# Kernel optimization log

Measured on AMD Instinct MI355X. Metric: run time of the kernel, lower is better.

Reference implementation:

```python
import jax, jax.numpy as jnp
import numpy as np

NUM_HEADS = 16
HEAD_DIM = 64  # hidden_size 1024 / 16 heads


def setup_inputs() -> dict:
    key = jax.random.key(0)
    ks = jax.random.split(key, 4)
    B, S, H = 2, 2048, 1024
    scale = 0.02
    return {
        "hidden_states": jax.random.normal(ks[0], (B, S, H), jnp.float32),
        "attention_mask": jnp.zeros((B, 1, 1, S), jnp.float32),  # additive mask
        "Wq": jax.random.normal(ks[1], (H, H), jnp.float32) * scale,
        "bq": jnp.zeros((H,), jnp.float32),
        "Wk": jax.random.normal(ks[2], (H, H), jnp.float32) * scale,
        "bk": jnp.zeros((H,), jnp.float32),
        "Wv": jax.random.normal(ks[3], (H, H), jnp.float32) * scale,
        "bv": jnp.zeros((H,), jnp.float32),
    }


def _split_heads(x):
    B, S, H = x.shape
    return x.reshape(B, S, NUM_HEADS, HEAD_DIM).transpose(0, 2, 1, 3)  # [B,h,S,dh]


def reference(hidden_states, attention_mask, Wq, bq, Wk, bk, Wv, bv):
    q = _split_heads(hidden_states @ Wq + bq)
    k = _split_heads(hidden_states @ Wk + bk)
    v = _split_heads(hidden_states @ Wv + bv)
    # scaled dot-product scores [B,h,S,S]
    scores = jnp.einsum("bhqd,bhkd->bhqk", q, k) / np.sqrt(HEAD_DIM).astype(np.float32)
    scores = scores + attention_mask  # additive mask, broadcast [B,1,1,S]
    probs = jax.nn.softmax(scores, axis=-1)  # dropout prob = 0.0
    ctx = jnp.einsum("bhqk,bhkd->bhqd", probs, v)
    B, h, S, dh = ctx.shape
    return ctx.transpose(0, 2, 1, 3).reshape(B, S, h * dh)  # [B,S,hidden]
```

## Files before the change

### kernel.cpp

```cpp
#include <hip/hip_runtime.h>
#include <hip/hip_bf16.h>


typedef __bf16 bf16x8 __attribute__((ext_vector_type(8)));
typedef __bf16 bf16x4 __attribute__((ext_vector_type(4)));
typedef float f32x4 __attribute__((ext_vector_type(4)));
typedef float f32x16 __attribute__((ext_vector_type(16)));
typedef int i32x4 __attribute__((ext_vector_type(4)));

static constexpr int H = 1024;
static constexpr int S = 2048;
static constexpr int NH = 16;
static constexpr int DH = 64;
static constexpr float L2E = 1.4426950408889634f;

#if __has_builtin(__builtin_amdgcn_exp2f)
#define EXP2F(x) __builtin_amdgcn_exp2f(x)
#else
#define EXP2F(x) __builtin_exp2f(x)
#endif

__device__ inline void gll16(const void* g, void* l) {
  __builtin_amdgcn_global_load_lds(
      (const __attribute__((address_space(1))) void*)g,
      (__attribute__((address_space(3))) void*)l, 16, 0, 0);
}

__device__ inline int pack2bf(float lo, float hi) {
  unsigned short a = __builtin_bit_cast(unsigned short, (__bf16)lo);
  unsigned short b = __builtin_bit_cast(unsigned short, (__bf16)hi);
  return (int)(((unsigned)b << 16) | (unsigned)a);
}

__device__ inline void plswap(int& a, int& b) {
  asm volatile("v_permlane32_swap_b32 %0, %1" : "+v"(a), "+v"(b));
}

__global__ __launch_bounds__(256) void convert_kernel(
    const float* __restrict__ X, const float* __restrict__ W0,
    const float* __restrict__ W1, const float* __restrict__ W2,
    __bf16* __restrict__ Xb, __bf16* __restrict__ Wt) {
  __shared__ float T[64][65];
  const int bid = blockIdx.x, tid = threadIdx.x;
  if (bid < 2048) {
    size_t i = ((size_t)bid * 256 + tid) * 8;
    float4 f0 = *(const float4*)(X + i);
    float4 f1 = *(const float4*)(X + i + 4);
    bf16x8 o;
    o[0] = (__bf16)f0.x; o[1] = (__bf16)f0.y; o[2] = (__bf16)f0.z; o[3] = (__bf16)f0.w;
    o[4] = (__bf16)f1.x; o[5] = (__bf16)f1.y; o[6] = (__bf16)f1.z; o[7] = (__bf16)f1.w;
    *(bf16x8*)(Xb + i) = o;
    return;
  }
  const int wid = bid - 2048;
  const int z = wid >> 8, t = wid & 255;
  const int k0 = (t >> 4) * 64, n0 = (t & 15) * 64;
  const float* W = z == 0 ? W0 : (z == 1 ? W1 : W2);
  __bf16* Wo = Wt + (size_t)z * H * H;
#pragma unroll
  for (int it = 0; it < 4; ++it) {
    int r = it * 16 + (tid >> 4), c = (tid & 15) * 4;
    *(float4*)&T[r][c] = *(const float4*)&W[(size_t)(k0 + r) * H + n0 + c];
  }
  __syncthreads();
#pragma unroll
  for (int it = 0; it < 4; ++it) {
    int n = it * 16 + (tid >> 4), c0 = (tid & 15) * 4;
    bf16x4 o;
#pragma unroll
    for (int j = 0; j < 4; ++j) o[j] = (__bf16)T[c0 + j][n];
    *(bf16x4*)&Wo[(size_t)(n0 + n) * H + k0 + c0] = o;
  }
}

__global__ __launch_bounds__(256, 3) void qkv_gemm_kernel(
    const __bf16* __restrict__ Xb, const __bf16* __restrict__ Wt,
    const float* __restrict__ bq, const float* __restrict__ bk,
    const float* __restrict__ bv,
    __bf16* __restrict__ Qt, __bf16* __restrict__ K, __bf16* __restrict__ Vt)
{
  __shared__ __bf16 As[128 * 64];
  __shared__ __bf16 Bs[128 * 64];

  const int tid = threadIdx.x, lane = tid & 63, w = tid >> 6;
  const int quad = lane >> 4, l16 = lane & 15;

  const int lin = blockIdx.x + 24 * blockIdx.y;
  const int swz = (lin & 7) * 96 + (lin >> 3);
  const int bx = swz >> 5;
  const int by = swz & 31;
  const int wsel = bx >> 3;
  const int n0 = (bx & 7) * 128;
  const int m0 = by * 128;
  const int wr = w & 1, wc = w >> 1;

  const __bf16* Wsel = Wt + (size_t)wsel * H * H;
  const float* bias = wsel == 0 ? bq : (wsel == 1 ? bk : bv);

  const __bf16* aptr[4];
  const __bf16* bptr[4];
#pragma unroll
  for (int i = 0; i < 4; ++i) {
    int s = w * 256 + i * 64 + lane;
    int row = s >> 3, col = s & 7, sc = col ^ (row & 7);
    aptr[i] = Xb + (size_t)(m0 + row) * H + sc * 8;
    bptr[i] = Wsel + (size_t)(n0 + row) * H + sc * 8;
  }

  f32x4 acc[4][4] = {};

  for (int k0 = 0; k0 < H; k0 += 64) {
    __syncthreads();
#pragma unroll
    for (int i = 0; i < 4; ++i) {
      gll16(aptr[i] + k0, &As[(w * 256 + i * 64) * 8]);
      gll16(bptr[i] + k0, &Bs[(w * 256 + i * 64) * 8]);
    }
    __syncthreads();
#pragma unroll
    for (int kc = 0; kc < 2; ++kc) {
      bf16x8 af[4], bfr[4];
#pragma unroll
      for (int t = 0; t < 4; ++t) {
        int ra = wr * 64 + t * 16 + l16;
        af[t] = *(const bf16x8*)&As[ra * 64 + (((kc * 4 + quad) ^ (ra & 7)) * 8)];
        int rb = wc * 64 + t * 16 + l16;
        bfr[t] = *(const bf16x8*)&Bs[rb * 64 + (((kc * 4 + quad) ^ (rb & 7)) * 8)];
      }
#pragma unroll
      for (int t = 0; t < 4; ++t)
#pragma unroll
        for (int u = 0; u < 4; ++u)
          acc[t][u] = __builtin_amdgcn_mfma_f32_16x16x32_bf16(af[t], bfr[u], acc[t][u], 0, 0, 0);
    }
  }

  const float qscale = 0.125f * L2E;
#pragma unroll
  for (int u = 0; u < 4; ++u) {
    int n = n0 + wc * 64 + u * 16 + l16;
    int head = n >> 6, d = n & 63;
    float bias_v = bias[n];
#pragma unroll
    for (int t = 0; t < 4; ++t) {
      int srow = m0 + wr * 64 + t * 16 + quad * 4;
      int b = srow >> 11, si = srow & (S - 1);
      int bh = b * NH + head;
      if (wsel == 1) {
        __bf16* dst = K + ((size_t)bh * S + si) * DH + d;
#pragma unroll
        for (int r = 0; r < 4; ++r)
          dst[(size_t)r * DH] = (__bf16)(acc[t][u][r] + bias_v);
      } else {
        float scl = wsel == 0 ? qscale : 1.0f;
        __bf16* outp = wsel == 0 ? Qt : Vt;
        bf16x4 o;
#pragma unroll
        for (int r = 0; r < 4; ++r) o[r] = (__bf16)((acc[t][u][r] + bias_v) * scl);
        *(bf16x4*)&outp[((size_t)bh * DH + d) * S + si] = o;
      }
    }
  }
}

__global__ __launch_bounds__(512, 4) void attn_kernel(
    const __bf16* __restrict__ Qt, const __bf16* __restrict__ K,
    const __bf16* __restrict__ Vt, const float* __restrict__ mask,
    float* __restrict__ out)
{
  __shared__ __bf16 SM[20480];
  __bf16* Ksb = SM;
  __bf16* Vsb = SM + 8192;
  float*  Ms  = (float*)(SM + 16384);

  const int tid = threadIdx.x, lane = tid & 63, w = tid >> 6;
  const int l31 = lane & 31, hi = lane >> 5;
  const int wl = w & 3, wh = w >> 2;

  const int lin = blockIdx.y * 16 + blockIdx.x;
  const int v = (lin & 7) * 64 + (lin >> 3);
  const int bh = v >> 4, b = bh >> 4, h = bh & 15;
  const int q0 = (v & 15) * 128;

  const __bf16* Qb = Qt + (size_t)bh * DH * S;
  const __bf16* Kb = K + (size_t)bh * S * DH;
  const __bf16* Vb = Vt + (size_t)bh * DH * S;
  const float* mb = mask + (size_t)b * S;

  {
    int idx = tid * 4;
    float4 mv = *(const float4*)&mb[idx];
    float4 sv = {mv.x * L2E, mv.y * L2E, mv.z * L2E, mv.w * L2E};
    *(float4*)&Ms[idx] = sv;
  }

  const int q = q0 + wl * 32 + l31;
  bf16x8 qf[4];
#pragma unroll
  for (int kc = 0; kc < 4; ++kc)
#pragma unroll
    for (int j = 0; j < 8; ++j)
      qf[kc][j] = Qb[(size_t)(kc * 16 + hi * 8 + j) * S + q];

  const int kvbase = wh * 1024;
  const __bf16* kptr[2];
  const __bf16* vptr[2];
#pragma unroll
  for (int i = 0; i < 2; ++i) {
    int s = wl * 128 + i * 64 + lane;
    int row = s >> 3, col = s & 7, sc = col ^ (row & 7);
    kptr[i] = Kb + (size_t)(kvbase + row) * DH + sc * 8;
    vptr[i] = Vb + (size_t)row * S + kvbase + sc * 8;
  }

  f32x16 o0 = {}, o1 = {};
  float dl = 0.0f;

  for (int st = 0; st < 16; ++st) {
    __syncthreads();
#pragma unroll
    for (int i = 0; i < 2; ++i) {
      gll16(kptr[i] + (size_t)st * 64 * DH,
            &Ksb[wh * 4096 + (wl * 128 + i * 64 + lane) * 8]);
      gll16(vptr[i] + st * 64,
            &Vsb[wh * 4096 + (wl * 128 + i * 64 + lane) * 8]);
    }
    __syncthreads();
    const __bf16* Kc = &Ksb[wh * 4096];
    const __bf16* Vc = &Vsb[wh * 4096];
    const int kvabs = kvbase + st * 64;

#pragma unroll
    for (int kvsub = 0; kvsub < 2; ++kvsub) {
      const int rk = kvsub * 32 + l31;
      f32x16 cc;
#pragma unroll
      for (int g = 0; g < 4; ++g) {
        float4 m4 = *(const float4*)&Ms[kvabs + kvsub * 32 + g * 8 + hi * 4];
        cc[4 * g + 0] = m4.x; cc[4 * g + 1] = m4.y;
        cc[4 * g + 2] = m4.z; cc[4 * g + 3] = m4.w;
      }
      __builtin_amdgcn_s_setprio(1);
#pragma unroll
      for (int kc = 0; kc < 4; ++kc) {
        bf16x8 af = *(const bf16x8*)&Kc[rk * 64 + (((kc * 2 + hi) ^ (l31 & 7)) * 8)];
        cc = __builtin_amdgcn_mfma_f32_32x32x16_bf16(af, qf[kc], cc, 0, 0, 0);
      }
      __builtin_amdgcn_s_setprio(0);

      float p[16];
#pragma unroll
      for (int r = 0; r < 16; ++r) { p[r] = EXP2F(cc[r]); dl += p[r]; }
      int a0 = pack2bf(p[0],  p[1]),  b0 = pack2bf(p[2],  p[3]);
      int a1 = pack2bf(p[4],  p[5]),  b1 = pack2bf(p[6],  p[7]);
      int a2 = pack2bf(p[8],  p[9]),  b2 = pack2bf(p[10], p[11]);
      int a3 = pack2bf(p[12], p[13]), b3 = pack2bf(p[14], p[15]);
      plswap(a0, a1); plswap(b0, b1);
      plswap(a2, a3); plswap(b2, b3);
      i32x4 pi0 = {a0, b0, a1, b1};
      i32x4 pi1 = {a2, b2, a3, b3};
      bf16x8 pf0 = __builtin_bit_cast(bf16x8, pi0);
      bf16x8 pf1 = __builtin_bit_cast(bf16x8, pi1);

      __builtin_amdgcn_s_setprio(1);
#pragma unroll
      for (int pp = 0; pp < 2; ++pp) {
        const int pc = kvsub * 2 + pp;
        const bf16x8 pf = pp ? pf1 : pf0;
        bf16x8 vf0 = *(const bf16x8*)&Vc[l31 * 64 + (((pc * 2 + hi) ^ (l31 & 7)) * 8)];
        o0 = __builtin_amdgcn_mfma_f32_32x32x16_bf16(vf0, pf, o0, 0, 0, 0);
        bf16x8 vf1 = *(const bf16x8*)&Vc[(32 + l31) * 64 + (((pc * 2 + hi) ^ (l31 & 7)) * 8)];
        o1 = __builtin_amdgcn_mfma_f32_32x32x16_bf16(vf1, pf, o1, 0, 0, 0);
      }
      __builtin_amdgcn_s_setprio(0);
    }
  }

  float lsum = dl + __shfl_xor(dl, 32);

  __syncthreads();
  float* Os = (float*)SM;
  float* Ls = Ms;
  if (wh == 1) {
#pragma unroll
    for (int g = 0; g < 4; ++g) {
      int s0 = (2 * g + hi) ^ (l31 & 7);
      float4 t0 = {o0[4 * g + 0], o0[4 * g + 1], o0[4 * g + 2], o0[4 * g + 3]};
      *(float4*)&Os[(wl * 32 + l31) * 64 + s0 * 4] = t0;
      int s1 = (8 + 2 * g + hi) ^ (l31 & 7);
      float4 t1 = {o1[4 * g + 0], o1[4 * g + 1], o1[4 * g + 2], o1[4 * g + 3]};
      *(float4*)&Os[(wl * 32 + l31) * 64 + s1 * 4] = t1;
    }
    if (hi == 0) Ls[wl * 32 + l31] = lsum;
  }
  __syncthreads();
  if (wh == 0) {
    float ltot = lsum + Ls[wl * 32 + l31];
    float invl = 1.0f / ltot;
#pragma unroll
    for (int g = 0; g < 4; ++g) {
      int d0 = g * 8 + hi * 4;
      int s0 = (2 * g + hi) ^ (l31 & 7);
      float4 u0 = *(const float4*)&Os[(wl * 32 + l31) * 64 + s0 * 4];
      float4 r0 = {(o0[4 * g + 0] + u0.x) * invl, (o0[4 * g + 1] + u0.y) * invl,
                   (o0[4 * g + 2] + u0.z) * invl, (o0[4 * g + 3] + u0.w) * invl};
      *(float4*)&out[((size_t)b * S + q) * H + h * DH + d0] = r0;
      int s1 = (8 + 2 * g + hi) ^ (l31 & 7);
      float4 u1 = *(const float4*)&Os[(wl * 32 + l31) * 64 + s1 * 4];
      float4 r1 = {(o1[4 * g + 0] + u1.x) * invl, (o1[4 * g + 1] + u1.y) * invl,
                   (o1[4 * g + 2] + u1.z) * invl, (o1[4 * g + 3] + u1.w) * invl};
      *(float4*)&out[((size_t)b * S + q) * H + h * DH + 32 + d0] = r1;
    }
  }
}

extern "C" void kernel_launch(void* const* d_in, const int* in_sizes, int n_in,
                              void* d_out, int out_size, void* d_ws, size_t ws_size,
                              hipStream_t stream) {
  const float* X    = (const float*)d_in[0];
  const float* mask = (const float*)d_in[1];
  const float* Wq   = (const float*)d_in[2];
  const float* bq   = (const float*)d_in[3];
  const float* Wk   = (const float*)d_in[4];
  const float* bk   = (const float*)d_in[5];
  const float* Wv   = (const float*)d_in[6];
  const float* bv   = (const float*)d_in[7];
  float* out = (float*)d_out;

  const size_t per = (size_t)2 * NH * S * DH;
  __bf16* Qws  = (__bf16*)d_ws;
  __bf16* Kws  = Qws + per;
  __bf16* Vtws = Kws + per;

  __bf16* Xb = (__bf16*)d_out;
  __bf16* Wt = Xb + per;

  convert_kernel<<<2816, 256, 0, stream>>>(X, Wq, Wk, Wv, Xb, Wt);
  qkv_gemm_kernel<<<dim3(24, 32), 256, 0, stream>>>(Xb, Wt, bq, bk, bv,
                                                    Qws, Kws, Vtws);
  attn_kernel<<<dim3(16, 32), 512, 0, stream>>>(Qws, Kws, Vtws, mask, out);
}
```

Before: 162.5 us.

## Fold exp(mask) into V and compute softmax row sums via MFMA

The additive mask is rewritten as a multiplicative factor: exp(mask) is precomputed once in the convert kernel, multiplied into V in the QKV GEMM epilogue, and dropped from score initialisation in attention. The per-element VALU accumulation of the softmax denominator is replaced by an extra MFMA whose A operand holds the exp(mask) vector in a single row. This removes the mask reads from LDS and sixteen adds per subtile, at the cost of one more MFMA per P·V step. It also stores exp(mask) in bf16, which loses precision for non-trivial masks.

```diff
diff --git a/kernel.cpp b/kernel.cpp
--- a/kernel.cpp
+++ b/kernel.cpp
@@ -39,7 +39,9 @@
 __global__ __launch_bounds__(256) void convert_kernel(
     const float* __restrict__ X, const float* __restrict__ W0,
     const float* __restrict__ W1, const float* __restrict__ W2,
-    __bf16* __restrict__ Xb, __bf16* __restrict__ Wt) {
+    const float* __restrict__ mask,
+    __bf16* __restrict__ Xb, __bf16* __restrict__ Wt,
+    float* __restrict__ EX) {
   __shared__ float T[64][65];
   const int bid = blockIdx.x, tid = threadIdx.x;
   if (bid < 2048) {
@@ -52,6 +54,17 @@
     *(bf16x8*)(Xb + i) = o;
     return;
   }
+  if (bid >= 2816) {
+#pragma unroll
+    for (int i = 0; i < 4; ++i) {
+      int idx = i * 1024 + tid * 4;
+      float4 mv = *(const float4*)&mask[idx];
+      float4 ev = {EXP2F(mv.x * L2E), EXP2F(mv.y * L2E),
+                   EXP2F(mv.z * L2E), EXP2F(mv.w * L2E)};
+      *(float4*)&EX[idx] = ev;
+    }
+    return;
+  }
   const int wid = bid - 2048;
   const int z = wid >> 8, t = wid & 255;
   const int k0 = (t >> 4) * 64, n0 = (t & 15) * 64;
@@ -76,7 +89,7 @@
 __global__ __launch_bounds__(256, 3) void qkv_gemm_kernel(
     const __bf16* __restrict__ Xb, const __bf16* __restrict__ Wt,
     const float* __restrict__ bq, const float* __restrict__ bk,
-    const float* __restrict__ bv,
+    const float* __restrict__ bv, const float* __restrict__ EX,
     __bf16* __restrict__ Qt, __bf16* __restrict__ K, __bf16* __restrict__ Vt)
 {
   __shared__ __bf16 As[128 * 64];
@@ -151,13 +164,19 @@
 #pragma unroll
         for (int r = 0; r < 4; ++r)
           dst[(size_t)r * DH] = (__bf16)(acc[t][u][r] + bias_v);
+      } else if (wsel == 0) {
+        bf16x4 o;
+#pragma unroll
+        for (int r = 0; r < 4; ++r) o[r] = (__bf16)((acc[t][u][r] + bias_v) * qscale);
+        *(bf16x4*)&Qt[((size_t)bh * DH + d) * S + si] = o;
       } else {
-        float scl = wsel == 0 ? qscale : 1.0f;
-        __bf16* outp = wsel == 0 ? Qt : Vt;
+        float4 em = *(const float4*)&EX[b * S + si];
         bf16x4 o;
-#pragma unroll
-        for (int r = 0; r < 4; ++r) o[r] = (__bf16)((acc[t][u][r] + bias_v) * scl);
-        *(bf16x4*)&outp[((size_t)bh * DH + d) * S + si] = o;
+        o[0] = (__bf16)((acc[t][u][0] + bias_v) * em.x);
+        o[1] = (__bf16)((acc[t][u][1] + bias_v) * em.y);
+        o[2] = (__bf16)((acc[t][u][2] + bias_v) * em.z);
+        o[3] = (__bf16)((acc[t][u][3] + bias_v) * em.w);
+        *(bf16x4*)&Vt[((size_t)bh * DH + d) * S + si] = o;
       }
     }
   }
@@ -165,13 +184,13 @@
 
 __global__ __launch_bounds__(512, 4) void attn_kernel(
     const __bf16* __restrict__ Qt, const __bf16* __restrict__ K,
-    const __bf16* __restrict__ Vt, const float* __restrict__ mask,
+    const __bf16* __restrict__ Vt, const float* __restrict__ EX,
     float* __restrict__ out)
 {
-  __shared__ __bf16 SM[20480];
+  __shared__ __bf16 SM[18432];
   __bf16* Ksb = SM;
   __bf16* Vsb = SM + 8192;
-  float*  Ms  = (float*)(SM + 16384);
+  __bf16* Es  = SM + 16384;
 
   const int tid = threadIdx.x, lane = tid & 63, w = tid >> 6;
   const int l31 = lane & 31, hi = lane >> 5;
@@ -185,13 +204,15 @@
   const __bf16* Qb = Qt + (size_t)bh * DH * S;
   const __bf16* Kb = K + (size_t)bh * S * DH;
   const __bf16* Vb = Vt + (size_t)bh * DH * S;
-  const float* mb = mask + (size_t)b * S;
+  const float* exb = EX + (size_t)b * S;
 
   {
     int idx = tid * 4;
-    float4 mv = *(const float4*)&mb[idx];
-    float4 sv = {mv.x * L2E, mv.y * L2E, mv.z * L2E, mv.w * L2E};
-    *(float4*)&Ms[idx] = sv;
+    float4 ev = *(const float4*)&exb[idx];
+    bf16x4 eb;
+    eb[0] = (__bf16)ev.x; eb[1] = (__bf16)ev.y;
+    eb[2] = (__bf16)ev.z; eb[3] = (__bf16)ev.w;
+    *(bf16x4*)&Es[idx] = eb;
   }
 
   const int q = q0 + wl * 32 + l31;
@@ -214,7 +235,8 @@
   }
 
   f32x16 o0 = {}, o1 = {};
-  float dl = 0.0f;
+  f32x16 o4 = {};
+  const bf16x8 zf = {};
 
   for (int st = 0; st < 16; ++st) {
     __syncthreads();
@@ -233,13 +255,7 @@
 #pragma unroll
     for (int kvsub = 0; kvsub < 2; ++kvsub) {
       const int rk = kvsub * 32 + l31;
-      f32x16 cc;
-#pragma unroll
-      for (int g = 0; g < 4; ++g) {
-        float4 m4 = *(const float4*)&Ms[kvabs + kvsub * 32 + g * 8 + hi * 4];
-        cc[4 * g + 0] = m4.x; cc[4 * g + 1] = m4.y;
-        cc[4 * g + 2] = m4.z; cc[4 * g + 3] = m4.w;
-      }
+      f32x16 cc = {};
       __builtin_amdgcn_s_setprio(1);
 #pragma unroll
       for (int kc = 0; kc < 4; ++kc) {
@@ -250,7 +266,7 @@
 
       float p[16];
 #pragma unroll
-      for (int r = 0; r < 16; ++r) { p[r] = EXP2F(cc[r]); dl += p[r]; }
+      for (int r = 0; r < 16; ++r) p[r] = EXP2F(cc[r]);
       int a0 = pack2bf(p[0],  p[1]),  b0 = pack2bf(p[2],  p[3]);
       int a1 = pack2bf(p[4],  p[5]),  b1 = pack2bf(p[6],  p[7]);
       int a2 = pack2bf(p[8],  p[9]),  b2 = pack2bf(p[10], p[11]);
@@ -271,16 +287,19 @@
         o0 = __builtin_amdgcn_mfma_f32_32x32x16_bf16(vf0, pf, o0, 0, 0, 0);
         bf16x8 vf1 = *(const bf16x8*)&Vc[(32 + l31) * 64 + (((pc * 2 + hi) ^ (l31 & 7)) * 8)];
         o1 = __builtin_amdgcn_mfma_f32_32x32x16_bf16(vf1, pf, o1, 0, 0, 0);
+        bf16x8 em = *(const bf16x8*)&Es[kvabs + pc * 16 + hi * 8];
+        bf16x8 afm = (l31 == 0) ? em : zf;
+        o4 = __builtin_amdgcn_mfma_f32_32x32x16_bf16(afm, pf, o4, 0, 0, 0);
       }
       __builtin_amdgcn_s_setprio(0);
     }
   }
 
-  float lsum = dl + __shfl_xor(dl, 32);
+  float lsum = __shfl(o4[0], l31, 64);
 
   __syncthreads();
   float* Os = (float*)SM;
-  float* Ls = Ms;
+  float* Ls = (float*)(SM + 16384);
   if (wh == 1) {
 #pragma unroll
     for (int g = 0; g < 4; ++g) {
@@ -331,12 +350,13 @@
   __bf16* Qws  = (__bf16*)d_ws;
   __bf16* Kws  = Qws + per;
   __bf16* Vtws = Kws + per;
+  float*  EXws = (float*)(Vtws + per);
 
   __bf16* Xb = (__bf16*)d_out;
   __bf16* Wt = Xb + per;
 
-  convert_kernel<<<2816, 256, 0, stream>>>(X, Wq, Wk, Wv, Xb, Wt);
-  qkv_gemm_kernel<<<dim3(24, 32), 256, 0, stream>>>(Xb, Wt, bq, bk, bv,
+  convert_kernel<<<2817, 256, 0, stream>>>(X, Wq, Wk, Wv, mask, Xb, Wt, EXws);
+  qkv_gemm_kernel<<<dim3(24, 32), 256, 0, stream>>>(Xb, Wt, bq, bk, bv, EXws,
                                                     Qws, Kws, Vtws);
-  attn_kernel<<<dim3(16, 32), 512, 0, stream>>>(Qws, Kws, Vtws, mask, out);
-}
+  attn_kernel<<<dim3(16, 32), 512, 0, stream>>>(Qws, Kws, Vtws, EXws, out);
+}
```

Result: slower. 166.1 us (+2.2%).

## Double KV tile size and software-pipeline QK with softmax-PV across sub-tiles

Applied to the files above, without the earlier changes.

Each loop step now loads a 128-wide KV tile per half-block instead of 64, which halves the number of barrier pairs, and widens the V swizzle to 16 columns. Inside a step, the QK MFMA for sub-tile n+1 is issued before the exp/pack/PV of sub-tile n, so tensor-core work overlaps the transcendental and pack work. LDS use grows from about 40KB to about 72KB per block, which may cut occupancy below the launch-bound target of 4 blocks, and keeping two score accumulators live adds register pressure.

```diff
diff --git a/kernel.cpp b/kernel.cpp
--- a/kernel.cpp
+++ b/kernel.cpp
@@ -168,10 +168,10 @@
     const __bf16* __restrict__ Vt, const float* __restrict__ mask,
     float* __restrict__ out)
 {
-  __shared__ __bf16 SM[20480];
+  __shared__ __bf16 SM[36864];
   __bf16* Ksb = SM;
-  __bf16* Vsb = SM + 8192;
-  float*  Ms  = (float*)(SM + 16384);
+  __bf16* Vsb = SM + 16384;
+  float*  Ms  = (float*)(SM + 32768);
 
   const int tid = threadIdx.x, lane = tid & 63, w = tid >> 6;
   const int l31 = lane & 31, hi = lane >> 5;
@@ -203,84 +203,100 @@
       qf[kc][j] = Qb[(size_t)(kc * 16 + hi * 8 + j) * S + q];
 
   const int kvbase = wh * 1024;
-  const __bf16* kptr[2];
-  const __bf16* vptr[2];
-#pragma unroll
-  for (int i = 0; i < 2; ++i) {
-    int s = wl * 128 + i * 64 + lane;
-    int row = s >> 3, col = s & 7, sc = col ^ (row & 7);
-    kptr[i] = Kb + (size_t)(kvbase + row) * DH + sc * 8;
-    vptr[i] = Vb + (size_t)row * S + kvbase + sc * 8;
+  int kof[4], vof[4];
+#pragma unroll
+  for (int i = 0; i < 4; ++i) {
+    int s = wl * 256 + i * 64 + lane;
+    {
+      int row = s >> 3, col = s & 7, sc = col ^ (row & 7);
+      kof[i] = (kvbase + row) * DH + sc * 8;
+    }
+    {
+      int row = s >> 4, col = s & 15, sc = col ^ (row & 15);
+      vof[i] = row * S + kvbase + sc * 8;
+    }
   }
 
   f32x16 o0 = {}, o1 = {};
   float dl = 0.0f;
 
-  for (int st = 0; st < 16; ++st) {
+#define QKSTEP(CC, KS)                                                        \
+  do {                                                                        \
+    const int rk_ = (KS) * 32 + l31;                                          \
+    _Pragma("unroll") for (int g = 0; g < 4; ++g) {                           \
+      float4 m4_ = *(const float4*)&Ms[kvabs + (KS) * 32 + g * 8 + hi * 4];   \
+      (CC)[4 * g + 0] = m4_.x; (CC)[4 * g + 1] = m4_.y;                       \
+      (CC)[4 * g + 2] = m4_.z; (CC)[4 * g + 3] = m4_.w;                       \
+    }                                                                         \
+    __builtin_amdgcn_s_setprio(1);                                            \
+    _Pragma("unroll") for (int kc = 0; kc < 4; ++kc) {                        \
+      bf16x8 af_ = *(const bf16x8*)&Kc[rk_ * 64 +                             \
+                                       (((kc * 2 + hi) ^ (rk_ & 7)) * 8)];    \
+      (CC) = __builtin_amdgcn_mfma_f32_32x32x16_bf16(af_, qf[kc], (CC),       \
+                                                     0, 0, 0);                \
+    }                                                                         \
+    __builtin_amdgcn_s_setprio(0);                                            \
+  } while (0)
+
+#define SMPV(CC, KS)                                                          \
+  do {                                                                        \
+    float p_[16];                                                             \
+    _Pragma("unroll") for (int r = 0; r < 16; ++r) {                          \
+      p_[r] = EXP2F((CC)[r]); dl += p_[r];                                    \
+    }                                                                         \
+    int a0_ = pack2bf(p_[0], p_[1]),   b0_ = pack2bf(p_[2], p_[3]);           \
+    int a1_ = pack2bf(p_[4], p_[5]),   b1_ = pack2bf(p_[6], p_[7]);           \
+    int a2_ = pack2bf(p_[8], p_[9]),   b2_ = pack2bf(p_[10], p_[11]);         \
+    int a3_ = pack2bf(p_[12], p_[13]), b3_ = pack2bf(p_[14], p_[15]);         \
+    plswap(a0_, a1_); plswap(b0_, b1_);                                       \
+    plswap(a2_, a3_); plswap(b2_, b3_);                                       \
+    i32x4 pi0_ = {a0_, b0_, a1_, b1_};                                        \
+    i32x4 pi1_ = {a2_, b2_, a3_, b3_};                                        \
+    bf16x8 pf0_ = __builtin_bit_cast(bf16x8, pi0_);                           \
+    bf16x8 pf1_ = __builtin_bit_cast(bf16x8, pi1_);                           \
+    __builtin_amdgcn_s_setprio(1);                                            \
+    _Pragma("unroll") for (int pp = 0; pp < 2; ++pp) {                        \
+      const int pc_ = (KS) * 2 + pp;                                          \
+      const bf16x8 pf_ = pp ? pf1_ : pf0_;                                    \
+      bf16x8 vf0_ = *(const bf16x8*)&Vc[l31 * 128 +                           \
+                                        (((pc_ * 2 + hi) ^ (l31 & 15)) * 8)]; \
+      o0 = __builtin_amdgcn_mfma_f32_32x32x16_bf16(vf0_, pf_, o0, 0, 0, 0);   \
+      bf16x8 vf1_ = *(const bf16x8*)&Vc[(32 + l31) * 128 +                    \
+                                        (((pc_ * 2 + hi) ^ (l31 & 15)) * 8)]; \
+      o1 = __builtin_amdgcn_mfma_f32_32x32x16_bf16(vf1_, pf_, o1, 0, 0, 0);   \
+    }                                                                         \
+    __builtin_amdgcn_s_setprio(0);                                            \
+  } while (0)
+
+  for (int st = 0; st < 8; ++st) {
     __syncthreads();
 #pragma unroll
-    for (int i = 0; i < 2; ++i) {
-      gll16(kptr[i] + (size_t)st * 64 * DH,
-            &Ksb[wh * 4096 + (wl * 128 + i * 64 + lane) * 8]);
-      gll16(vptr[i] + st * 64,
-            &Vsb[wh * 4096 + (wl * 128 + i * 64 + lane) * 8]);
+    for (int i = 0; i < 4; ++i) {
+      gll16(Kb + kof[i] + st * 128 * DH,
+            &Ksb[wh * 8192 + (wl * 256 + i * 64 + lane) * 8]);
+      gll16(Vb + vof[i] + st * 128,
+            &Vsb[wh * 8192 + (wl * 256 + i * 64 + lane) * 8]);
     }
     __syncthreads();
-    const __bf16* Kc = &Ksb[wh * 4096];
-    const __bf16* Vc = &Vsb[wh * 4096];
-    const int kvabs = kvbase + st * 64;
-
-#pragma unroll
-    for (int kvsub = 0; kvsub < 2; ++kvsub) {
-      const int rk = kvsub * 32 + l31;
-      f32x16 cc;
-#pragma unroll
-      for (int g = 0; g < 4; ++g) {
-        float4 m4 = *(const float4*)&Ms[kvabs + kvsub * 32 + g * 8 + hi * 4];
-        cc[4 * g + 0] = m4.x; cc[4 * g + 1] = m4.y;
-        cc[4 * g + 2] = m4.z; cc[4 * g + 3] = m4.w;
-      }
-      __builtin_amdgcn_s_setprio(1);
-#pragma unroll
-      for (int kc = 0; kc < 4; ++kc) {
-        bf16x8 af = *(const bf16x8*)&Kc[rk * 64 + (((kc * 2 + hi) ^ (l31 & 7)) * 8)];
-        cc = __builtin_amdgcn_mfma_f32_32x32x16_bf16(af, qf[kc], cc, 0, 0, 0);
-      }
-      __builtin_amdgcn_s_setprio(0);
-
-      float p[16];
-#pragma unroll
-      for (int r = 0; r < 16; ++r) { p[r] = EXP2F(cc[r]); dl += p[r]; }
-      int a0 = pack2bf(p[0],  p[1]),  b0 = pack2bf(p[2],  p[3]);
-      int a1 = pack2bf(p[4],  p[5]),  b1 = pack2bf(p[6],  p[7]);
-      int a2 = pack2bf(p[8],  p[9]),  b2 = pack2bf(p[10], p[11]);
-      int a3 = pack2bf(p[12], p[13]), b3 = pack2bf(p[14], p[15]);
-      plswap(a0, a1); plswap(b0, b1);
-      plswap(a2, a3); plswap(b2, b3);
-      i32x4 pi0 = {a0, b0, a1, b1};
-      i32x4 pi1 = {a2, b2, a3, b3};
-      bf16x8 pf0 = __builtin_bit_cast(bf16x8, pi0);
-      bf16x8 pf1 = __builtin_bit_cast(bf16x8, pi1);
-
-      __builtin_amdgcn_s_setprio(1);
-#pragma unroll
-      for (int pp = 0; pp < 2; ++pp) {
-        const int pc = kvsub * 2 + pp;
-        const bf16x8 pf = pp ? pf1 : pf0;
-        bf16x8 vf0 = *(const bf16x8*)&Vc[l31 * 64 + (((pc * 2 + hi) ^ (l31 & 7)) * 8)];
-        o0 = __builtin_amdgcn_mfma_f32_32x32x16_bf16(vf0, pf, o0, 0, 0, 0);
-        bf16x8 vf1 = *(const bf16x8*)&Vc[(32 + l31) * 64 + (((pc * 2 + hi) ^ (l31 & 7)) * 8)];
-        o1 = __builtin_amdgcn_mfma_f32_32x32x16_bf16(vf1, pf, o1, 0, 0, 0);
-      }
-      __builtin_amdgcn_s_setprio(0);
-    }
-  }
+    const __bf16* Kc = &Ksb[wh * 8192];
+    const __bf16* Vc = &Vsb[wh * 8192];
+    const int kvabs = kvbase + st * 128;
+
+    f32x16 ccA, ccB;
+    QKSTEP(ccA, 0);
+    QKSTEP(ccB, 1); SMPV(ccA, 0);
+    QKSTEP(ccA, 2); SMPV(ccB, 1);
+    QKSTEP(ccB, 3); SMPV(ccA, 2);
+    SMPV(ccB, 3);
+  }
+#undef QKSTEP
+#undef SMPV
 
   float lsum = dl + __shfl_xor(dl, 32);
 
   __syncthreads();
   float* Os = (float*)SM;
-  float* Ls = Ms;
+  float* Ls = (float*)(SM + 32768);
   if (wh == 1) {
 #pragma unroll
     for (int g = 0; g < 4; ++g) {
```

Measured after the change: 211.3 us. +30.0%, slower.

## Load K/V MFMA fragments directly from global memory instead of LDS staging

Applied to the files above, without the earlier changes.

Removes the LDS staging of K and V tiles and the two block barriers per iteration. Each wave now reads its MFMA operand fragments straight from global memory (through L1/L2) in 32-key steps. This drops the barrier stalls and LDS traffic, but the four query waves sharing a KV half now each fetch the same K/V data from cache, and there is no explicit prefetch to hide global latency.

```diff
diff --git a/kernel.cpp b/kernel.cpp
--- a/kernel.cpp
+++ b/kernel.cpp
@@ -169,9 +169,7 @@
     float* __restrict__ out)
 {
   __shared__ __bf16 SM[20480];
-  __bf16* Ksb = SM;
-  __bf16* Vsb = SM + 8192;
-  float*  Ms  = (float*)(SM + 16384);
+  float* Ms = (float*)(SM + 16384);
 
   const int tid = threadIdx.x, lane = tid & 63, w = tid >> 6;
   const int l31 = lane & 31, hi = lane >> 5;
@@ -202,78 +200,62 @@
     for (int j = 0; j < 8; ++j)
       qf[kc][j] = Qb[(size_t)(kc * 16 + hi * 8 + j) * S + q];
 
+  __syncthreads();
+
   const int kvbase = wh * 1024;
-  const __bf16* kptr[2];
-  const __bf16* vptr[2];
-#pragma unroll
-  for (int i = 0; i < 2; ++i) {
-    int s = wl * 128 + i * 64 + lane;
-    int row = s >> 3, col = s & 7, sc = col ^ (row & 7);
-    kptr[i] = Kb + (size_t)(kvbase + row) * DH + sc * 8;
-    vptr[i] = Vb + (size_t)row * S + kvbase + sc * 8;
-  }
+  const __bf16* kp  = Kb + (size_t)(kvbase + l31) * DH + hi * 8;
+  const __bf16* vp0 = Vb + (size_t)l31 * S + kvbase + hi * 8;
+  const __bf16* vp1 = vp0 + (size_t)32 * S;
 
   f32x16 o0 = {}, o1 = {};
   float dl = 0.0f;
 
-  for (int st = 0; st < 16; ++st) {
-    __syncthreads();
-#pragma unroll
-    for (int i = 0; i < 2; ++i) {
-      gll16(kptr[i] + (size_t)st * 64 * DH,
-            &Ksb[wh * 4096 + (wl * 128 + i * 64 + lane) * 8]);
-      gll16(vptr[i] + st * 64,
-            &Vsb[wh * 4096 + (wl * 128 + i * 64 + lane) * 8]);
-    }
-    __syncthreads();
-    const __bf16* Kc = &Ksb[wh * 4096];
-    const __bf16* Vc = &Vsb[wh * 4096];
-    const int kvabs = kvbase + st * 64;
-
-#pragma unroll
-    for (int kvsub = 0; kvsub < 2; ++kvsub) {
-      const int rk = kvsub * 32 + l31;
-      f32x16 cc;
-#pragma unroll
-      for (int g = 0; g < 4; ++g) {
-        float4 m4 = *(const float4*)&Ms[kvabs + kvsub * 32 + g * 8 + hi * 4];
-        cc[4 * g + 0] = m4.x; cc[4 * g + 1] = m4.y;
-        cc[4 * g + 2] = m4.z; cc[4 * g + 3] = m4.w;
-      }
-      __builtin_amdgcn_s_setprio(1);
-#pragma unroll
-      for (int kc = 0; kc < 4; ++kc) {
-        bf16x8 af = *(const bf16x8*)&Kc[rk * 64 + (((kc * 2 + hi) ^ (l31 & 7)) * 8)];
-        cc = __builtin_amdgcn_mfma_f32_32x32x16_bf16(af, qf[kc], cc, 0, 0, 0);
-      }
-      __builtin_amdgcn_s_setprio(0);
-
-      float p[16];
-#pragma unroll
-      for (int r = 0; r < 16; ++r) { p[r] = EXP2F(cc[r]); dl += p[r]; }
-      int a0 = pack2bf(p[0],  p[1]),  b0 = pack2bf(p[2],  p[3]);
-      int a1 = pack2bf(p[4],  p[5]),  b1 = pack2bf(p[6],  p[7]);
-      int a2 = pack2bf(p[8],  p[9]),  b2 = pack2bf(p[10], p[11]);
-      int a3 = pack2bf(p[12], p[13]), b3 = pack2bf(p[14], p[15]);
-      plswap(a0, a1); plswap(b0, b1);
-      plswap(a2, a3); plswap(b2, b3);
-      i32x4 pi0 = {a0, b0, a1, b1};
-      i32x4 pi1 = {a2, b2, a3, b3};
-      bf16x8 pf0 = __builtin_bit_cast(bf16x8, pi0);
-      bf16x8 pf1 = __builtin_bit_cast(bf16x8, pi1);
-
-      __builtin_amdgcn_s_setprio(1);
-#pragma unroll
-      for (int pp = 0; pp < 2; ++pp) {
-        const int pc = kvsub * 2 + pp;
-        const bf16x8 pf = pp ? pf1 : pf0;
-        bf16x8 vf0 = *(const bf16x8*)&Vc[l31 * 64 + (((pc * 2 + hi) ^ (l31 & 7)) * 8)];
-        o0 = __builtin_amdgcn_mfma_f32_32x32x16_bf16(vf0, pf, o0, 0, 0, 0);
-        bf16x8 vf1 = *(const bf16x8*)&Vc[(32 + l31) * 64 + (((pc * 2 + hi) ^ (l31 & 7)) * 8)];
-        o1 = __builtin_amdgcn_mfma_f32_32x32x16_bf16(vf1, pf, o1, 0, 0, 0);
-      }
-      __builtin_amdgcn_s_setprio(0);
-    }
+  for (int ks = 0; ks < 32; ++ks) {
+    const int kvabs = kvbase + ks * 32;
+
+    f32x16 cc;
+#pragma unroll
+    for (int g = 0; g < 4; ++g) {
+      float4 m4 = *(const float4*)&Ms[kvabs + g * 8 + hi * 4];
+      cc[4 * g + 0] = m4.x; cc[4 * g + 1] = m4.y;
+      cc[4 * g + 2] = m4.z; cc[4 * g + 3] = m4.w;
+    }
+    bf16x8 af[4], vfa[2], vfb[2];
+#pragma unroll
+    for (int kc = 0; kc < 4; ++kc)
+      af[kc] = *(const bf16x8*)&kp[(size_t)ks * 32 * DH + kc * 16];
+#pragma unroll
+    for (int pc = 0; pc < 2; ++pc) {
+      vfa[pc] = *(const bf16x8*)&vp0[ks * 32 + pc * 16];
+      vfb[pc] = *(const bf16x8*)&vp1[ks * 32 + pc * 16];
+    }
+
+    __builtin_amdgcn_s_setprio(1);
+#pragma unroll
+    for (int kc = 0; kc < 4; ++kc)
+      cc = __builtin_amdgcn_mfma_f32_32x32x16_bf16(af[kc], qf[kc], cc, 0, 0, 0);
+    __builtin_amdgcn_s_setprio(0);
+
+    float p[16];
+#pragma unroll
+    for (int r = 0; r < 16; ++r) { p[r] = EXP2F(cc[r]); dl += p[r]; }
+    int a0 = pack2bf(p[0],  p[1]),  b0 = pack2bf(p[2],  p[3]);
+    int a1 = pack2bf(p[4],  p[5]),  b1 = pack2bf(p[6],  p[7]);
+    int a2 = pack2bf(p[8],  p[9]),  b2 = pack2bf(p[10], p[11]);
+    int a3 = pack2bf(p[12], p[13]), b3 = pack2bf(p[14], p[15]);
+    plswap(a0, a1); plswap(b0, b1);
+    plswap(a2, a3); plswap(b2, b3);
+    i32x4 pi0 = {a0, b0, a1, b1};
+    i32x4 pi1 = {a2, b2, a3, b3};
+    bf16x8 pf0 = __builtin_bit_cast(bf16x8, pi0);
+    bf16x8 pf1 = __builtin_bit_cast(bf16x8, pi1);
+
+    __builtin_amdgcn_s_setprio(1);
+    o0 = __builtin_amdgcn_mfma_f32_32x32x16_bf16(vfa[0], pf0, o0, 0, 0, 0);
+    o1 = __builtin_amdgcn_mfma_f32_32x32x16_bf16(vfb[0], pf0, o1, 0, 0, 0);
+    o0 = __builtin_amdgcn_mfma_f32_32x32x16_bf16(vfa[1], pf1, o0, 0, 0, 0);
+    o1 = __builtin_amdgcn_mfma_f32_32x32x16_bf16(vfb[1], pf1, o1, 0, 0, 0);
+    __builtin_amdgcn_s_setprio(0);
   }
 
   float lsum = dl + __shfl_xor(dl, 32);
```

New measurement: 233.1 us. 1.43x slower.
